# Kernel optimization log

Measured on AMD Instinct MI355X. Metric: run time of the kernel, lower is better.

## Reference

```python
import jax, jax.numpy as jnp
import numpy as np

V, D, C, NUM_CLASSES = 50000, 128, 128, 200
N, S = 4096, 128
NUM_VIDEOS = 256
KSIZES = (3, 4, 5)


def setup_inputs() -> dict:
    key = jax.random.key(0)
    ks = jax.random.split(key, 10)
    input_x = jax.random.randint(ks[0], (N, 1, S), 0, V)
    # sorted segment ids, every video non-empty (contiguous ragged segments)
    segment_ids = ((jnp.arange(N) * NUM_VIDEOS) // N).astype(jnp.int32)
    emb = jax.random.normal(ks[1], (V, D), dtype=jnp.float32) * (2.0 / (V + D)) ** 0.5  # xavier_normal
    W3 = jax.random.normal(ks[2], (3, D, C), dtype=jnp.float32) * 0.05
    b3 = jnp.zeros((C,), dtype=jnp.float32)
    W4 = jax.random.normal(ks[3], (4, D, C), dtype=jnp.float32) * 0.05
    b4 = jnp.zeros((C,), dtype=jnp.float32)
    W5 = jax.random.normal(ks[4], (5, D, C), dtype=jnp.float32) * 0.05
    b5 = jnp.zeros((C,), dtype=jnp.float32)
    Wout = jax.random.normal(ks[5], (3 * C, NUM_CLASSES), dtype=jnp.float32) * 0.05
    bout = jnp.zeros((NUM_CLASSES,), dtype=jnp.float32)
    return {"input_x": input_x, "segment_ids": segment_ids, "emb": emb,
            "W3": W3, "b3": b3, "W4": W4, "b4": b4, "W5": W5, "b5": b5,
            "Wout": Wout, "bout": bout}


def _conv_maxpool(x, W, b):
    # x: [N, S, D], W: [w, D, C] -> conv over time (VALID), then max over time -> [N, C]
    y = jax.lax.conv_general_dilated(x, W, window_strides=(1,), padding='VALID',
                                     dimension_numbers=('NWC', 'WIO', 'NWC')) + b
    return jnp.max(y, axis=1)


def reference(input_x, segment_ids, emb, W3, b3, W4, b4, W5, b5, Wout, bout):
    x = emb[input_x[:, 0, :]]                       # [N, S, D]
    feat = jnp.concatenate([_conv_maxpool(x, W3, b3),
                            _conv_maxpool(x, W4, b4),
                            _conv_maxpool(x, W5, b5)], axis=1)  # [N, 3C]
    logits = feat @ Wout + bout                     # [N, num_classes]
    scores = jax.nn.sigmoid(logits)
    # ragged per-video max over contiguous text rows
    video_scores = jax.ops.segment_max(scores, segment_ids, num_segments=NUM_VIDEOS)
    return video_scores
```

## Files before the change

kernel.cpp:

```cpp
#include <hip/hip_runtime.h>
#include <hip/hip_bf16.h>


using bf16_t  = __bf16;
using bf16x4  = __attribute__((ext_vector_type(4))) __bf16;
using bf16x8  = __attribute__((ext_vector_type(8))) __bf16;
using floatx4 = __attribute__((ext_vector_type(4))) float;

#define N_SENT 4096
#define S_LEN  128
#define D_DIM  128
#define C_DIM  128
#define NCLS   200
#define NVID   256
#define V_SZ   50000

#define X_ROWS   132
#define X_STRIDE 136

#define BP3_OFF 0
#define BP4_OFF 49152
#define BP5_OFF 114688
#define BPACK_ELEMS 196608

#define FEAT_OFF  (1u << 20)
#define EMB16_OFF (8u << 20)

__global__ void prep_emb(const float* __restrict__ emb, bf16_t* __restrict__ emb16) {
  int i4 = blockIdx.x * 256 + threadIdx.x;
  const floatx4 f = __builtin_nontemporal_load((const floatx4*)emb + i4);
  bf16x4 h;
  h.x = (bf16_t)f.x; h.y = (bf16_t)f.y; h.z = (bf16_t)f.z; h.w = (bf16_t)f.w;
  __builtin_nontemporal_store(h, (bf16x4*)emb16 + i4);
}

__global__ void prep_bpack(const float* __restrict__ W3,
                           const float* __restrict__ W4,
                           const float* __restrict__ W5,
                           bf16_t* __restrict__ bpack) {
  int idx = blockIdx.x * 256 + threadIdx.x;
  if (idx >= BPACK_ELEMS) return;
  int KS; const float* W; int rel;
  if (idx < BP4_OFF)      { KS = 3; W = W3; rel = idx; }
  else if (idx < BP5_OFF) { KS = 4; W = W4; rel = idx - BP4_OFF; }
  else                    { KS = 5; W = W5; rel = idx - BP5_OFF; }
  int szct  = 2048 * KS;
  int ctile = rel / szct;
  int r2    = rel - ctile * szct;
  int g     = r2 >> 7;
  int r3    = r2 & 127;
  int n     = r3 >> 3;
  int j     = r3 & 7;
  bpack[idx] = (bf16_t)W[(g * 8 + j) * C_DIM + (ctile * 16 + n)];
}

template <int KS>
__device__ __forceinline__ void conv_k(const bf16_t* Xs_lane,
                                       const bf16_t* bp0, const bf16_t* bp1,
                                       const float* __restrict__ bk,
                                       float* __restrict__ feat,
                                       int m, int q, int lane, int sent,
                                       int koff, int ct0) {
  floatx4 acc[2][8];
#pragma unroll
  for (int ct = 0; ct < 2; ++ct)
#pragma unroll
    for (int mt = 0; mt < 8; ++mt)
      acc[ct][mt] = (floatx4){0.f, 0.f, 0.f, 0.f};

  const bf16_t* Arow = Xs_lane;

#pragma unroll 1
  for (int c0 = 0; c0 < KS; ++c0) {
    bf16x8 bfr0[4], bfr1[4];
#pragma unroll
    for (int st = 0; st < 4; ++st) {
      bfr0[st] = *(const bf16x8*)(bp0 + st * 512);
      bfr1[st] = *(const bf16x8*)(bp1 + st * 512);
    }
    bp0 += 2048;
    bp1 += 2048;
#pragma unroll
    for (int mt = 0; mt < 8; ++mt) {
#pragma unroll
      for (int st = 0; st < 4; ++st) {
        const bf16x8 a = *(const bf16x8*)(Arow + mt * 16 * X_STRIDE + st * 32);
        acc[0][mt] = __builtin_amdgcn_mfma_f32_16x16x32_bf16(a, bfr0[st], acc[0][mt], 0, 0, 0);
        acc[1][mt] = __builtin_amdgcn_mfma_f32_16x16x32_bf16(a, bfr1[st], acc[1][mt], 0, 0, 0);
      }
    }
    Arow += X_STRIDE;
  }

  const int tlim = S_LEN - KS + 1;
#pragma unroll
  for (int ct = 0; ct < 2; ++ct) {
    float mx = -__builtin_inff();
#pragma unroll
    for (int mt = 0; mt < 8; ++mt)
#pragma unroll
      for (int r = 0; r < 4; ++r) {
        const int t = mt * 16 + q * 4 + r;
        if (t < tlim) mx = fmaxf(mx, acc[ct][mt][r]);
      }
    mx = fmaxf(mx, __shfl_xor(mx, 16));
    mx = fmaxf(mx, __shfl_xor(mx, 32));
    const int c = (ct0 + ct) * 16 + m;
    if (lane < 16)
      __builtin_nontemporal_store(mx + bk[c], &feat[sent * 384 + koff + c]);
  }
}

__global__ __launch_bounds__(256, 3) void conv_gemm(
    const int* __restrict__ input_x, const bf16_t* __restrict__ emb16,
    const bf16_t* __restrict__ bpack, const float* __restrict__ b3,
    const float* __restrict__ b4, const float* __restrict__ b5,
    float* __restrict__ feat) {
  __shared__ __align__(16) bf16_t Xs[X_ROWS * X_STRIDE];
  const int sent = blockIdx.x;
  const int tid  = threadIdx.x;

  {
    const int rip = tid >> 4;
    const int l16 = tid & 15;
#pragma unroll
    for (int r0 = 0; r0 < S_LEN; r0 += 16) {
      const int row   = r0 + rip;
      const int token = __builtin_nontemporal_load(&input_x[sent * S_LEN + row]);
      const bf16x8 v  =
          __builtin_nontemporal_load((const bf16x8*)(emb16 + token * D_DIM + l16 * 8));
      *(bf16x8*)(&Xs[row * X_STRIDE + l16 * 8]) = v;
    }
    for (int i = tid; i < 4 * X_STRIDE; i += 256)
      Xs[128 * X_STRIDE + i] = (bf16_t)0.f;
  }
  __syncthreads();

  const int wv   = tid >> 6;
  const int lane = tid & 63;
  const int m    = lane & 15;
  const int q    = lane >> 4;
  const bf16_t* Xs_lane = Xs + m * X_STRIDE + q * 8;
  const int     ct0     = 2 * wv;
  const int     blaneoff = q * 128 + m * 8;

  conv_k<3>(Xs_lane, bpack + BP3_OFF + (ct0 + 0) * (2048 * 3) + blaneoff,
            bpack + BP3_OFF + (ct0 + 1) * (2048 * 3) + blaneoff,
            b3, feat, m, q, lane, sent, 0, ct0);
  __builtin_amdgcn_sched_barrier(0);
  conv_k<4>(Xs_lane, bpack + BP4_OFF + (ct0 + 0) * (2048 * 4) + blaneoff,
            bpack + BP4_OFF + (ct0 + 1) * (2048 * 4) + blaneoff,
            b4, feat, m, q, lane, sent, 128, ct0);
  __builtin_amdgcn_sched_barrier(0);
  conv_k<5>(Xs_lane, bpack + BP5_OFF + (ct0 + 0) * (2048 * 5) + blaneoff,
            bpack + BP5_OFF + (ct0 + 1) * (2048 * 5) + blaneoff,
            b5, feat, m, q, lane, sent, 256, ct0);
}

__global__ void classify(const float* __restrict__ feat,
                         const float* __restrict__ Wout,
                         const float* __restrict__ bout,
                         float* __restrict__ out) {
  __shared__ float fs[16 * 384];
  const int vid = blockIdx.x;
  const int tid = threadIdx.x;
  for (int i = tid; i < 16 * 384; i += 256) fs[i] = feat[vid * 16 * 384 + i];
  __syncthreads();
  if (tid < NCLS) {
    float acc[16];
#pragma unroll
    for (int s = 0; s < 16; ++s) acc[s] = 0.f;
    for (int d = 0; d < 384; ++d) {
      const float wv = Wout[d * NCLS + tid];
#pragma unroll
      for (int s = 0; s < 16; ++s) acc[s] = fmaf(fs[s * 384 + d], wv, acc[s]);
    }
    const float b = bout[tid];
    float vmax = -__builtin_inff();
#pragma unroll
    for (int s = 0; s < 16; ++s) {
      const float sc = 1.f / (1.f + __expf(-(acc[s] + b)));
      vmax = fmaxf(vmax, sc);
    }
    out[vid * NCLS + tid] = vmax;
  }
}

extern "C" void kernel_launch(void* const* d_in, const int* in_sizes, int n_in,
                              void* d_out, int out_size, void* d_ws, size_t ws_size,
                              hipStream_t stream) {
  const int*   input_x = (const int*)d_in[0];
  const float* emb  = (const float*)d_in[2];
  const float* W3   = (const float*)d_in[3];
  const float* b3   = (const float*)d_in[4];
  const float* W4   = (const float*)d_in[5];
  const float* b4   = (const float*)d_in[6];
  const float* W5   = (const float*)d_in[7];
  const float* b5   = (const float*)d_in[8];
  const float* Wout = (const float*)d_in[9];
  const float* bout = (const float*)d_in[10];

  bf16_t* bpack = (bf16_t*)d_ws;
  float*  feat  = (float*)((char*)d_ws + FEAT_OFF);
  bf16_t* emb16 = (bf16_t*)((char*)d_ws + EMB16_OFF);
  float*  out   = (float*)d_out;

  prep_emb<<<(V_SZ * D_DIM) / 4 / 256, 256, 0, stream>>>(emb, emb16);
  prep_bpack<<<BPACK_ELEMS / 256, 256, 0, stream>>>(W3, W4, W5, bpack);
  conv_gemm<<<N_SENT, 256, 0, stream>>>(input_x, emb16, bpack, b3, b4, b5, feat);
  classify<<<NVID, 256, 0, stream>>>(feat, Wout, bout, out);
}
```

Measured before the change: 289.7 us.

## Fuse three conv widths into one pass sharing A-fragment LDS loads across time halves

Restructures the conv GEMM so the three kernel widths share each A-fragment LDS read. The time axis is split into two 64-row halves to keep accumulator registers bounded, with shared shift steps for all widths and trailing steps for widths 4 and 5. This cuts LDS traffic on the A operand roughly threefold. The cost is more live accumulators and B-fragment registers, which may pressure the 3-block occupancy target or cause spills.

```diff
diff --git a/kernel.cpp b/kernel.cpp
--- a/kernel.cpp
+++ b/kernel.cpp
@@ -22,6 +22,9 @@
 #define BP4_OFF 49152
 #define BP5_OFF 114688
 #define BPACK_ELEMS 196608
+#define BCT3 6144
+#define BCT4 8192
+#define BCT5 10240
 
 #define FEAT_OFF  (1u << 20)
 #define EMB16_OFF (8u << 20)
@@ -54,61 +57,98 @@
   bpack[idx] = (bf16_t)W[(g * 8 + j) * C_DIM + (ctile * 16 + n)];
 }
 
-template <int KS>
-__device__ __forceinline__ void conv_k(const bf16_t* Xs_lane,
-                                       const bf16_t* bp0, const bf16_t* bp1,
-                                       const float* __restrict__ bk,
-                                       float* __restrict__ feat,
-                                       int m, int q, int lane, int sent,
-                                       int koff, int ct0) {
-  floatx4 acc[2][8];
+template <bool DO3, bool DO4>
+__device__ __forceinline__ void kstep(const bf16_t* Arow,
+                                      const bf16_t* p3, const bf16_t* p4,
+                                      const bf16_t* p5,
+                                      floatx4 (&A3)[2][4], floatx4 (&A4)[2][4],
+                                      floatx4 (&A5)[2][4]) {
+#pragma unroll
+  for (int st = 0; st < 4; ++st) {
+    bf16x8 b5a = *(const bf16x8*)(p5 + st * 512);
+    bf16x8 b5b = *(const bf16x8*)(p5 + BCT5 + st * 512);
+    bf16x8 b4a, b4b, b3a, b3b;
+    if constexpr (DO4) {
+      b4a = *(const bf16x8*)(p4 + st * 512);
+      b4b = *(const bf16x8*)(p4 + BCT4 + st * 512);
+    }
+    if constexpr (DO3) {
+      b3a = *(const bf16x8*)(p3 + st * 512);
+      b3b = *(const bf16x8*)(p3 + BCT3 + st * 512);
+    }
+#pragma unroll
+    for (int mt = 0; mt < 4; ++mt) {
+      const bf16x8 a = *(const bf16x8*)(Arow + mt * 16 * X_STRIDE + st * 32);
+      A5[0][mt] = __builtin_amdgcn_mfma_f32_16x16x32_bf16(a, b5a, A5[0][mt], 0, 0, 0);
+      A5[1][mt] = __builtin_amdgcn_mfma_f32_16x16x32_bf16(a, b5b, A5[1][mt], 0, 0, 0);
+      if constexpr (DO4) {
+        A4[0][mt] = __builtin_amdgcn_mfma_f32_16x16x32_bf16(a, b4a, A4[0][mt], 0, 0, 0);
+        A4[1][mt] = __builtin_amdgcn_mfma_f32_16x16x32_bf16(a, b4b, A4[1][mt], 0, 0, 0);
+      }
+      if constexpr (DO3) {
+        A3[0][mt] = __builtin_amdgcn_mfma_f32_16x16x32_bf16(a, b3a, A3[0][mt], 0, 0, 0);
+        A3[1][mt] = __builtin_amdgcn_mfma_f32_16x16x32_bf16(a, b3b, A3[1][mt], 0, 0, 0);
+      }
+    }
+  }
+}
+
+template <int H, int KS>
+__device__ __forceinline__ void redmax(const floatx4 (&A)[2][4], int q,
+                                       float (&mx)[2]) {
+  const int tlim = S_LEN - KS + 1;
 #pragma unroll
   for (int ct = 0; ct < 2; ++ct)
 #pragma unroll
-    for (int mt = 0; mt < 8; ++mt)
-      acc[ct][mt] = (floatx4){0.f, 0.f, 0.f, 0.f};
-
-  const bf16_t* Arow = Xs_lane;
+    for (int mt = 0; mt < 4; ++mt)
+#pragma unroll
+      for (int r = 0; r < 4; ++r) {
+        const int t = H * 64 + mt * 16 + q * 4 + r;
+        if (H == 0 || t < S_LEN - 4)
+          mx[ct] = fmaxf(mx[ct], A[ct][mt][r]);
+        else if (t < tlim)
+          mx[ct] = fmaxf(mx[ct], A[ct][mt][r]);
+      }
+}
+
+template <int H>
+__device__ __forceinline__ void half_pass(const bf16_t* __restrict__ Xs,
+                                          const bf16_t* b3base,
+                                          const bf16_t* b4base,
+                                          const bf16_t* b5base,
+                                          int m, int q,
+                                          float (&mx3)[2], float (&mx4)[2],
+                                          float (&mx5)[2]) {
+  floatx4 A3[2][4], A4[2][4], A5[2][4];
+#pragma unroll
+  for (int ct = 0; ct < 2; ++ct)
+#pragma unroll
+    for (int mt = 0; mt < 4; ++mt) {
+      A3[ct][mt] = (floatx4){0.f, 0.f, 0.f, 0.f};
+      A4[ct][mt] = (floatx4){0.f, 0.f, 0.f, 0.f};
+      A5[ct][mt] = (floatx4){0.f, 0.f, 0.f, 0.f};
+    }
+
+  const bf16_t* Ah = Xs + (H * 64 + m) * X_STRIDE + q * 8;
+  const bf16_t* p3 = b3base;
+  const bf16_t* p4 = b4base;
+  const bf16_t* p5 = b5base;
 
 #pragma unroll 1
-  for (int c0 = 0; c0 < KS; ++c0) {
-    bf16x8 bfr0[4], bfr1[4];
-#pragma unroll
-    for (int st = 0; st < 4; ++st) {
-      bfr0[st] = *(const bf16x8*)(bp0 + st * 512);
-      bfr1[st] = *(const bf16x8*)(bp1 + st * 512);
-    }
-    bp0 += 2048;
-    bp1 += 2048;
-#pragma unroll
-    for (int mt = 0; mt < 8; ++mt) {
-#pragma unroll
-      for (int st = 0; st < 4; ++st) {
-        const bf16x8 a = *(const bf16x8*)(Arow + mt * 16 * X_STRIDE + st * 32);
-        acc[0][mt] = __builtin_amdgcn_mfma_f32_16x16x32_bf16(a, bfr0[st], acc[0][mt], 0, 0, 0);
-        acc[1][mt] = __builtin_amdgcn_mfma_f32_16x16x32_bf16(a, bfr1[st], acc[1][mt], 0, 0, 0);
-      }
-    }
-    Arow += X_STRIDE;
-  }
-
-  const int tlim = S_LEN - KS + 1;
-#pragma unroll
-  for (int ct = 0; ct < 2; ++ct) {
-    float mx = -__builtin_inff();
-#pragma unroll
-    for (int mt = 0; mt < 8; ++mt)
-#pragma unroll
-      for (int r = 0; r < 4; ++r) {
-        const int t = mt * 16 + q * 4 + r;
-        if (t < tlim) mx = fmaxf(mx, acc[ct][mt][r]);
-      }
-    mx = fmaxf(mx, __shfl_xor(mx, 16));
-    mx = fmaxf(mx, __shfl_xor(mx, 32));
-    const int c = (ct0 + ct) * 16 + m;
-    if (lane < 16)
-      __builtin_nontemporal_store(mx + bk[c], &feat[sent * 384 + koff + c]);
-  }
+  for (int c0 = 0; c0 < 3; ++c0) {
+    kstep<true, true>(Ah, p3, p4, p5, A3, A4, A5);
+    p3 += 2048; p4 += 2048; p5 += 2048; Ah += X_STRIDE;
+  }
+  __builtin_amdgcn_sched_barrier(0);
+  kstep<false, true>(Ah, p3, p4, p5, A3, A4, A5);
+  p5 += 2048; Ah += X_STRIDE;
+  __builtin_amdgcn_sched_barrier(0);
+  kstep<false, false>(Ah, p3, p4, p5, A3, A4, A5);
+  __builtin_amdgcn_sched_barrier(0);
+
+  redmax<H, 3>(A3, q, mx3);
+  redmax<H, 4>(A4, q, mx4);
+  redmax<H, 5>(A5, q, mx5);
 }
 
 __global__ __launch_bounds__(256, 3) void conv_gemm(
@@ -140,21 +180,34 @@
   const int lane = tid & 63;
   const int m    = lane & 15;
   const int q    = lane >> 4;
-  const bf16_t* Xs_lane = Xs + m * X_STRIDE + q * 8;
-  const int     ct0     = 2 * wv;
-  const int     blaneoff = q * 128 + m * 8;
-
-  conv_k<3>(Xs_lane, bpack + BP3_OFF + (ct0 + 0) * (2048 * 3) + blaneoff,
-            bpack + BP3_OFF + (ct0 + 1) * (2048 * 3) + blaneoff,
-            b3, feat, m, q, lane, sent, 0, ct0);
-  __builtin_amdgcn_sched_barrier(0);
-  conv_k<4>(Xs_lane, bpack + BP4_OFF + (ct0 + 0) * (2048 * 4) + blaneoff,
-            bpack + BP4_OFF + (ct0 + 1) * (2048 * 4) + blaneoff,
-            b4, feat, m, q, lane, sent, 128, ct0);
-  __builtin_amdgcn_sched_barrier(0);
-  conv_k<5>(Xs_lane, bpack + BP5_OFF + (ct0 + 0) * (2048 * 5) + blaneoff,
-            bpack + BP5_OFF + (ct0 + 1) * (2048 * 5) + blaneoff,
-            b5, feat, m, q, lane, sent, 256, ct0);
+  const int blaneoff = q * 128 + m * 8;
+
+  const bf16_t* b3base = bpack + BP3_OFF + 2 * wv * BCT3 + blaneoff;
+  const bf16_t* b4base = bpack + BP4_OFF + 2 * wv * BCT4 + blaneoff;
+  const bf16_t* b5base = bpack + BP5_OFF + 2 * wv * BCT5 + blaneoff;
+
+  float mx3[2] = {-__builtin_inff(), -__builtin_inff()};
+  float mx4[2] = {-__builtin_inff(), -__builtin_inff()};
+  float mx5[2] = {-__builtin_inff(), -__builtin_inff()};
+
+  half_pass<0>(Xs, b3base, b4base, b5base, m, q, mx3, mx4, mx5);
+  __builtin_amdgcn_sched_barrier(0);
+  half_pass<1>(Xs, b3base, b4base, b5base, m, q, mx3, mx4, mx5);
+
+  float* frow = feat + sent * 384;
+#pragma unroll
+  for (int ct = 0; ct < 2; ++ct) {
+    float v3 = mx3[ct], v4 = mx4[ct], v5 = mx5[ct];
+    v3 = fmaxf(v3, __shfl_xor(v3, 16)); v3 = fmaxf(v3, __shfl_xor(v3, 32));
+    v4 = fmaxf(v4, __shfl_xor(v4, 16)); v4 = fmaxf(v4, __shfl_xor(v4, 32));
+    v5 = fmaxf(v5, __shfl_xor(v5, 16)); v5 = fmaxf(v5, __shfl_xor(v5, 32));
+    const int c = (2 * wv + ct) * 16 + m;
+    if (lane < 16) {
+      __builtin_nontemporal_store(v3 + b3[c], &frow[c]);
+      __builtin_nontemporal_store(v4 + b4[c], &frow[128 + c]);
+      __builtin_nontemporal_store(v5 + b5[c], &frow[256 + c]);
+    }
+  }
 }
 
 __global__ void classify(const float* __restrict__ feat,
```

Result: slower. 513.7 us (+77.3%).
